# Performance work log

Hardware: AMD Instinct MI355X
Metric: run time of the kernel (lower is better)

The kernel has to match this reference:

```python
import jax, jax.numpy as jnp
import numpy as np

STRIDE = 1
PADDING = 1

def setup_inputs() -> dict:
    key = jax.random.key(0)
    k1, k2 = jax.random.split(key)
    x = jax.random.normal(k1, (32, 128, 56, 56), dtype=jnp.float32)
    # kaiming_uniform_(a=sqrt(5)) -> U(-bound, bound), bound = sqrt(6/((1+5)*fan_in)) = 1/sqrt(fan_in)
    fan_in = 128 * 3 * 3
    bound = 1.0 / np.sqrt(fan_in)
    weight = jax.random.uniform(k2, (256, 128, 3, 3), dtype=jnp.float32, minval=-bound, maxval=bound)
    bias = jnp.zeros((256,), dtype=jnp.float32)
    return {"x": x, "weight": weight, "bias": bias}

def reference(x, weight, bias):
    # Dense 2D convolution (cross-correlation, matching torch semantics), NCHW/OIHW.
    out = jax.lax.conv_general_dilated(
        x, weight,
        window_strides=(STRIDE, STRIDE),
        padding=[(PADDING, PADDING), (PADDING, PADDING)],
        dimension_numbers=("NCHW", "OIHW", "NCHW"),
    )
    return out + bias[None, :, None, None]
```

## Files before the change

### kernel.cpp

```cpp
#include <hip/hip_runtime.h>

typedef __bf16 bfvec8 __attribute__((ext_vector_type(8)));
typedef float f32x4 __attribute__((ext_vector_type(4)));
typedef unsigned short u16x8 __attribute__((ext_vector_type(8)));
typedef unsigned int u32;

constexpr int C_IN = 128, Wd = 56, Hd = 56, HW = 3136, K_OUT = 256, N_IMG = 32;
constexpr int KKTOT = 1152;
constexpr int WP = 58;
constexpr size_t XP_ELEMS = (size_t)N_IMG * WP * WP * C_IN;
constexpr size_t XP_BYTES = XP_ELEMS * 2;
constexpr size_t WT_ELEMS = (size_t)9 * 4 * 2 * 128 * 32;

constexpr int HALO_BLKS = 456;
constexpr int WT_BLKS   = 1152;
constexpr int XPOSE_BLKS = N_IMG * Hd;
constexpr int PREP_GRID = HALO_BLKS + WT_BLKS + XPOSE_BLKS;

__device__ inline unsigned short f2bf(float f) {
    union { float f; unsigned u; } v; v.f = f;
    unsigned u = v.u;
    u += 0x7fffu + ((u >> 16) & 1u);
    return (unsigned short)(u >> 16);
}

__device__ inline void gld16(const void* g, void* l) {
    __builtin_amdgcn_global_load_lds(
        (const __attribute__((address_space(1))) u32*)g,
        (__attribute__((address_space(3))) u32*)l, 16, 0, 0);
}

#define CFENCE() asm volatile("" ::: "memory")

__global__ __launch_bounds__(256) void prep(const float* __restrict__ x,
                                            const float* __restrict__ wgt,
                                            unsigned short* __restrict__ xp,
                                            unsigned short* __restrict__ wt) {
    __shared__ unsigned short T[Wd * C_IN];
    const int bx = blockIdx.x;

    if (bx < HALO_BLKS) {
        int v = bx * 256 + threadIdx.x;
        int n = v / 3648, rem = v - n * 3648;
        int p = rem >> 4, c8 = rem & 15;
        int hh, ww;
        if (p < 58)       { hh = 0;       ww = p;       }
        else if (p < 116) { hh = 57;      ww = p - 58;  }
        else if (p < 172) { hh = p - 115; ww = 0;       }
        else              { hh = p - 171; ww = 57;      }
        const u16x8 z = {0, 0, 0, 0, 0, 0, 0, 0};
        *(u16x8*)(xp + ((size_t)(n * WP + hh) * WP + ww) * C_IN + c8 * 8) = z;
        return;
    }
    if (bx < HALO_BLKS + WT_BLKS) {
        int o = (bx - HALO_BLKS) * 256 + threadIdx.x;
        int kk = o & 31, n = (o >> 5) & 127, nt = (o >> 12) & 1,
            ch = (o >> 13) & 3, rs = o >> 15;
        float v = wgt[(size_t)(nt * 128 + n) * KKTOT + (ch * 32 + kk) * 9 + rs];
        wt[o] = f2bf(v);
        return;
    }
    const int nb = bx - (HALO_BLKS + WT_BLKS);
    const int n = nb / Hd, h = nb - n * Hd;
    const float* src = x + (size_t)n * C_IN * HW + h * Wd;
    #pragma unroll
    for (int k = 0; k < 7; ++k) {
        int idx = threadIdx.x + k * 256;
        int c = idx / 14, w4 = idx - c * 14;
        const float4 v = *(const float4*)(src + (size_t)c * HW + w4 * 4);
        const int sw = (w4 & 15) * 8;
        T[(w4 * 4 + 0) * C_IN + (c ^ sw)] = f2bf(v.x);
        T[(w4 * 4 + 1) * C_IN + (c ^ sw)] = f2bf(v.y);
        T[(w4 * 4 + 2) * C_IN + (c ^ sw)] = f2bf(v.z);
        T[(w4 * 4 + 3) * C_IN + (c ^ sw)] = f2bf(v.w);
    }
    __syncthreads();
    unsigned short* dst = xp + ((size_t)(n * WP + h + 1) * WP + 1) * C_IN;
    const u16x8* s8 = (const u16x8*)T;
    u16x8* d8 = (u16x8*)dst;
    #pragma unroll
    for (int k = 0; k < 4; ++k) {
        int idx = threadIdx.x + k * 256;
        if (idx < 896) {
            int w = idx >> 4, j8 = idx & 15;
            d8[idx] = s8[w * 16 + (j8 ^ ((w >> 2) & 15))];
        }
    }
}

__global__ __launch_bounds__(256) void conv_gemm(
    const unsigned short* __restrict__ xp, const unsigned short* __restrict__ wt,
    const float* __restrict__ bias, float* __restrict__ out)
{
    __shared__ __align__(16) unsigned short As[3][128 * 32];

    const int tid = threadIdx.x;
    const int hbx = blockIdx.x;
    const int lbx = (hbx & 7) * 196 + (hbx >> 3);
    const int nt  = lbx & 1;
    const int mtile = (lbx >> 1) * 128;

    const int cg8 = ((tid & 3) ^ ((tid >> 3) & 3)) * 8;

    const unsigned short *gA0, *gA1;
    {
        int mrow = tid >> 2;
        int m = mtile + mrow;
        int ni = m / HW; int hw = m - ni * HW; int h = hw / Wd; int w = hw - h * Wd;
        gA0 = xp + ((size_t)(ni * WP + h + 1) * WP + (w + 1)) * C_IN + cg8;
        m += 64;
        ni = m / HW; hw = m - ni * HW; h = hw / Wd; w = hw - h * Wd;
        gA1 = xp + ((size_t)(ni * WP + h + 1) * WP + (w + 1)) * C_IN + cg8;
    }

    const int wave = tid >> 6, lane = tid & 63;
    const int wrow = (wave >> 1) * 64, wcol = (wave & 1) * 64;
    const int r16 = lane & 15, quad = lane >> 4;
    const int qsw = (quad ^ ((r16 >> 1) & 3)) * 8;

    const unsigned short* gBf = wt + (size_t)nt * 4096 + (wcol + r16) * 32 + quad * 8;

    const f32x4 zero4 = {0.f, 0.f, 0.f, 0.f};
    f32x4 acc[4][4];
    #pragma unroll
    for (int i = 0; i < 4; ++i)
        #pragma unroll
        for (int j = 0; j < 4; ++j)
            acc[i][j] = zero4;

    bfvec8 bf[2][4];

    auto issueA = [&](int step, int buf) {
        const int rs = step >> 2, ch = step & 3;
        const int dr = rs / 3 - 1, dc = rs % 3 - 1;
        const int aoff = (dr * WP + dc) * C_IN + ch * 32;
        gld16(gA0 + aoff, (void*)(As[buf] + tid * 8));
        gld16(gA1 + aoff, (void*)(As[buf] + 2048 + tid * 8));
    };
    auto loadB = [&](int step, int par) {
        #pragma unroll
        for (int ni = 0; ni < 4; ++ni)
            bf[par][ni] = *(const bfvec8*)(gBf + (size_t)step * 8192 + ni * 512);
    };

    issueA(0, 0);
    loadB(0, 0);
    issueA(1, 1);

    #pragma unroll
    for (int step = 0; step < 36; ++step) {
        const int cur = step % 3;
        const int par = step & 1;

        CFENCE(); __builtin_amdgcn_s_barrier(); CFENCE();
        if (step < 35) loadB(step + 1, par ^ 1);
        if (step < 34) issueA(step + 2, (step + 2) % 3);
        if (step < 34) {
            asm volatile("s_waitcnt vmcnt(8)" ::: "memory");
        } else if (step == 34) {
            asm volatile("s_waitcnt vmcnt(4)" ::: "memory");
        } else {
            asm volatile("s_waitcnt vmcnt(0)" ::: "memory");
        }
        CFENCE(); __builtin_amdgcn_s_barrier(); CFENCE();

        bfvec8 af[4];
        #pragma unroll
        for (int mi = 0; mi < 4; ++mi)
            af[mi] = *(const bfvec8*)&As[cur][(wrow + mi * 16 + r16) * 32 + qsw];

        #pragma unroll
        for (int mi = 0; mi < 4; ++mi)
            #pragma unroll
            for (int ni = 0; ni < 4; ++ni)
                acc[mi][ni] = __builtin_amdgcn_mfma_f32_16x16x32_bf16(
                    af[mi], bf[par][ni], acc[mi][ni], 0, 0, 0);
    }

    const int ntile = nt * 128;
    #pragma unroll
    for (int ni = 0; ni < 4; ++ni) {
        const int k = ntile + wcol + ni * 16 + r16;
        const float bb = bias[k];
        #pragma unroll
        for (int mi = 0; mi < 4; ++mi) {
            const int mb  = mtile + wrow + mi * 16 + quad * 4;
            const int ne  = mb / HW;
            const int hwe = mb - ne * HW;
            f32x4 v;
            #pragma unroll
            for (int i = 0; i < 4; ++i) v[i] = acc[mi][ni][i] + bb;
            *(f32x4*)(out + ((size_t)ne * K_OUT + k) * HW + hwe) = v;
        }
    }
}

extern "C" void kernel_launch(void* const* d_in, const int* in_sizes, int n_in,
                              void* d_out, int out_size, void* d_ws, size_t ws_size,
                              hipStream_t stream) {
    const float* x    = (const float*)d_in[0];
    const float* wgt  = (const float*)d_in[1];
    const float* bias = (const float*)d_in[2];
    float* out = (float*)d_out;

    unsigned short* xp = (unsigned short*)d_ws;
    unsigned short* wt = (unsigned short*)((char*)d_ws + XP_BYTES);

    prep<<<dim3(PREP_GRID), dim3(256), 0, stream>>>(x, wgt, xp, wt);
    conv_gemm<<<dim3(1568), dim3(256), 0, stream>>>(xp, wt, bias, out);
}
```

Baseline: 225.4 us.

## Enlarge GEMM tile to 256x128 and stage weights through LDS

Doubles the M tile per block from 128 to 256 rows, so each wave computes 128x64 with 8x4 MFMA accumulators, and halves the grid to 784 blocks. Weight tiles are now loaded into LDS with async global-to-LDS copies alongside the activations, instead of each wave loading them directly into registers. This is meant to increase arithmetic intensity and cut redundant weight fetches. In exchange it doubles accumulator registers and raises LDS use, with 784 blocks on 256 CUs risking uneven tail utilization.

After: 217.1 us. 1.04x faster.

```diff
diff --git a/kernel.cpp b/kernel.cpp
--- a/kernel.cpp
+++ b/kernel.cpp
@@ -88,93 +88,86 @@
     }
 }
 
-__global__ __launch_bounds__(256) void conv_gemm(
+__global__ __launch_bounds__(256, 2) void conv_gemm(
     const unsigned short* __restrict__ xp, const unsigned short* __restrict__ wt,
     const float* __restrict__ bias, float* __restrict__ out)
 {
-    __shared__ __align__(16) unsigned short As[3][128 * 32];
+    __shared__ __align__(16) unsigned short As[3][256 * 32];
+    __shared__ __align__(16) unsigned short Bs[3][128 * 32];
 
     const int tid = threadIdx.x;
     const int hbx = blockIdx.x;
-    const int lbx = (hbx & 7) * 196 + (hbx >> 3);
+    const int lbx = (hbx & 7) * 98 + (hbx >> 3);
     const int nt  = lbx & 1;
-    const int mtile = (lbx >> 1) * 128;
+    const int mtile = (lbx >> 1) * 256;
 
     const int cg8 = ((tid & 3) ^ ((tid >> 3) & 3)) * 8;
 
-    const unsigned short *gA0, *gA1;
-    {
-        int mrow = tid >> 2;
-        int m = mtile + mrow;
+    const unsigned short* gA[4];
+    #pragma unroll
+    for (int L = 0; L < 4; ++L) {
+        int m = mtile + L * 64 + (tid >> 2);
         int ni = m / HW; int hw = m - ni * HW; int h = hw / Wd; int w = hw - h * Wd;
-        gA0 = xp + ((size_t)(ni * WP + h + 1) * WP + (w + 1)) * C_IN + cg8;
-        m += 64;
-        ni = m / HW; hw = m - ni * HW; h = hw / Wd; w = hw - h * Wd;
-        gA1 = xp + ((size_t)(ni * WP + h + 1) * WP + (w + 1)) * C_IN + cg8;
-    }
+        gA[L] = xp + ((size_t)(ni * WP + h + 1) * WP + (w + 1)) * C_IN + cg8;
+    }
+    const unsigned short* gB = wt + (size_t)nt * 4096 + (size_t)(tid & 0xFC) * 8 + cg8;
 
     const int wave = tid >> 6, lane = tid & 63;
-    const int wrow = (wave >> 1) * 64, wcol = (wave & 1) * 64;
+    const int wrow = (wave >> 1) * 128, wcol = (wave & 1) * 64;
     const int r16 = lane & 15, quad = lane >> 4;
     const int qsw = (quad ^ ((r16 >> 1) & 3)) * 8;
 
-    const unsigned short* gBf = wt + (size_t)nt * 4096 + (wcol + r16) * 32 + quad * 8;
-
     const f32x4 zero4 = {0.f, 0.f, 0.f, 0.f};
-    f32x4 acc[4][4];
-    #pragma unroll
-    for (int i = 0; i < 4; ++i)
+    f32x4 acc[8][4];
+    #pragma unroll
+    for (int i = 0; i < 8; ++i)
         #pragma unroll
         for (int j = 0; j < 4; ++j)
             acc[i][j] = zero4;
 
-    bfvec8 bf[2][4];
-
-    auto issueA = [&](int step, int buf) {
+    auto issue = [&](int step, int buf) {
         const int rs = step >> 2, ch = step & 3;
         const int dr = rs / 3 - 1, dc = rs % 3 - 1;
         const int aoff = (dr * WP + dc) * C_IN + ch * 32;
-        gld16(gA0 + aoff, (void*)(As[buf] + tid * 8));
-        gld16(gA1 + aoff, (void*)(As[buf] + 2048 + tid * 8));
+        const size_t boff = (size_t)step * 8192;
+        #pragma unroll
+        for (int L = 0; L < 4; ++L)
+            gld16(gA[L] + aoff, (void*)(As[buf] + L * 2048 + tid * 8));
+        gld16(gB + boff,        (void*)(Bs[buf] + tid * 8));
+        gld16(gB + boff + 2048, (void*)(Bs[buf] + 2048 + tid * 8));
     };
-    auto loadB = [&](int step, int par) {
-        #pragma unroll
-        for (int ni = 0; ni < 4; ++ni)
-            bf[par][ni] = *(const bfvec8*)(gBf + (size_t)step * 8192 + ni * 512);
-    };
-
-    issueA(0, 0);
-    loadB(0, 0);
-    issueA(1, 1);
+
+    issue(0, 0);
+    issue(1, 1);
 
     #pragma unroll
     for (int step = 0; step < 36; ++step) {
         const int cur = step % 3;
-        const int par = step & 1;
 
         CFENCE(); __builtin_amdgcn_s_barrier(); CFENCE();
-        if (step < 35) loadB(step + 1, par ^ 1);
-        if (step < 34) issueA(step + 2, (step + 2) % 3);
         if (step < 34) {
-            asm volatile("s_waitcnt vmcnt(8)" ::: "memory");
+            issue(step + 2, (step + 2) % 3);
+            asm volatile("s_waitcnt vmcnt(12)" ::: "memory");
         } else if (step == 34) {
-            asm volatile("s_waitcnt vmcnt(4)" ::: "memory");
+            asm volatile("s_waitcnt vmcnt(6)" ::: "memory");
         } else {
             asm volatile("s_waitcnt vmcnt(0)" ::: "memory");
         }
         CFENCE(); __builtin_amdgcn_s_barrier(); CFENCE();
 
-        bfvec8 af[4];
-        #pragma unroll
-        for (int mi = 0; mi < 4; ++mi)
-            af[mi] = *(const bfvec8*)&As[cur][(wrow + mi * 16 + r16) * 32 + qsw];
-
-        #pragma unroll
-        for (int mi = 0; mi < 4; ++mi)
+        bfvec8 bf[4];
+        #pragma unroll
+        for (int ni = 0; ni < 4; ++ni)
+            bf[ni] = *(const bfvec8*)&Bs[cur][(wcol + ni * 16 + r16) * 32 + qsw];
+
+        #pragma unroll
+        for (int mi = 0; mi < 8; ++mi) {
+            const bfvec8 af = *(const bfvec8*)&As[cur][(wrow + mi * 16 + r16) * 32 + qsw];
             #pragma unroll
             for (int ni = 0; ni < 4; ++ni)
                 acc[mi][ni] = __builtin_amdgcn_mfma_f32_16x16x32_bf16(
-                    af[mi], bf[par][ni], acc[mi][ni], 0, 0, 0);
+                    af, bf[ni], acc[mi][ni], 0, 0, 0);
+        }
     }
 
     const int ntile = nt * 128;
@@ -183,7 +176,7 @@
         const int k = ntile + wcol + ni * 16 + r16;
         const float bb = bias[k];
         #pragma unroll
-        for (int mi = 0; mi < 4; ++mi) {
+        for (int mi = 0; mi < 8; ++mi) {
             const int mb  = mtile + wrow + mi * 16 + quad * 4;
             const int ne  = mb / HW;
             const int hwe = mb - ne * HW;
@@ -207,5 +200,5 @@
     unsigned short* wt = (unsigned short*)((char*)d_ws + XP_BYTES);
 
     prep<<<dim3(PREP_GRID), dim3(256), 0, stream>>>(x, wgt, xp, wt);
-    conv_gemm<<<dim3(1568), dim3(256), 0, stream>>>(xp, wt, bias, out);
-}
+    conv_gemm<<<dim3(784), dim3(256), 0, stream>>>(xp, wt, bias, out);
+}
```

## Stage weight tiles through LDS and double-buffer fragment reads ahead of MFMA

Applied to the files above, without the earlier changes.

The weight (B) operand was loaded per lane directly from global memory. It now goes through a triple-buffered LDS tile using async global_load_lds, matching how A is loaded. Fragments for the next step are read from LDS before the current step's MFMAs, and the MFMA block runs at raised wave priority via s_setprio. Launch bounds now request 3 blocks per SM. The goal is fewer redundant global B loads and better overlap of LDS reads with matrix math, at the cost of double the LDS footprint and more registers for the doubled A fragments.

Result: faster. 214.8 us (-4.7%).

```diff
diff --git a/kernel.cpp b/kernel.cpp
--- a/kernel.cpp
+++ b/kernel.cpp
@@ -88,11 +88,12 @@
     }
 }
 
-__global__ __launch_bounds__(256) void conv_gemm(
+__global__ __launch_bounds__(256, 3) void conv_gemm(
     const unsigned short* __restrict__ xp, const unsigned short* __restrict__ wt,
     const float* __restrict__ bias, float* __restrict__ out)
 {
     __shared__ __align__(16) unsigned short As[3][128 * 32];
+    __shared__ __align__(16) unsigned short Bs[3][128 * 32];
 
     const int tid = threadIdx.x;
     const int hbx = blockIdx.x;
@@ -112,14 +113,13 @@
         ni = m / HW; hw = m - ni * HW; h = hw / Wd; w = hw - h * Wd;
         gA1 = xp + ((size_t)(ni * WP + h + 1) * WP + (w + 1)) * C_IN + cg8;
     }
+    const unsigned short* gB = wt + (size_t)nt * 4096 + (size_t)(tid & 0xFC) * 8 + cg8;
 
     const int wave = tid >> 6, lane = tid & 63;
     const int wrow = (wave >> 1) * 64, wcol = (wave & 1) * 64;
     const int r16 = lane & 15, quad = lane >> 4;
     const int qsw = (quad ^ ((r16 >> 1) & 3)) * 8;
 
-    const unsigned short* gBf = wt + (size_t)nt * 4096 + (wcol + r16) * 32 + quad * 8;
-
     const f32x4 zero4 = {0.f, 0.f, 0.f, 0.f};
     f32x4 acc[4][4];
     #pragma unroll
@@ -128,53 +128,57 @@
         for (int j = 0; j < 4; ++j)
             acc[i][j] = zero4;
 
-    bfvec8 bf[2][4];
-
-    auto issueA = [&](int step, int buf) {
+    bfvec8 af[2][4], bf[2][4];
+
+    auto issue = [&](int step, int buf) {
         const int rs = step >> 2, ch = step & 3;
         const int dr = rs / 3 - 1, dc = rs % 3 - 1;
         const int aoff = (dr * WP + dc) * C_IN + ch * 32;
+        const size_t boff = (size_t)step * 8192;
         gld16(gA0 + aoff, (void*)(As[buf] + tid * 8));
         gld16(gA1 + aoff, (void*)(As[buf] + 2048 + tid * 8));
+        gld16(gB + boff,        (void*)(Bs[buf] + tid * 8));
+        gld16(gB + boff + 2048, (void*)(Bs[buf] + 2048 + tid * 8));
     };
-    auto loadB = [&](int step, int par) {
+    auto readFrags = [&](int step, int set) {
+        const int cur = step % 3;
+        #pragma unroll
+        for (int mi = 0; mi < 4; ++mi)
+            af[set][mi] = *(const bfvec8*)&As[cur][(wrow + mi * 16 + r16) * 32 + qsw];
         #pragma unroll
         for (int ni = 0; ni < 4; ++ni)
-            bf[par][ni] = *(const bfvec8*)(gBf + (size_t)step * 8192 + ni * 512);
+            bf[set][ni] = *(const bfvec8*)&Bs[cur][(wcol + ni * 16 + r16) * 32 + qsw];
     };
 
-    issueA(0, 0);
-    loadB(0, 0);
-    issueA(1, 1);
+    issue(0, 0);
+    issue(1, 1);
+    asm volatile("s_waitcnt vmcnt(4)" ::: "memory");
+    CFENCE(); __builtin_amdgcn_s_barrier(); CFENCE();
+    readFrags(0, 0);
 
     #pragma unroll
     for (int step = 0; step < 36; ++step) {
-        const int cur = step % 3;
         const int par = step & 1;
 
         CFENCE(); __builtin_amdgcn_s_barrier(); CFENCE();
-        if (step < 35) loadB(step + 1, par ^ 1);
-        if (step < 34) issueA(step + 2, (step + 2) % 3);
         if (step < 34) {
-            asm volatile("s_waitcnt vmcnt(8)" ::: "memory");
+            issue(step + 2, (step + 2) % 3);
+            asm volatile("s_waitcnt vmcnt(4)" ::: "memory");
         } else if (step == 34) {
-            asm volatile("s_waitcnt vmcnt(4)" ::: "memory");
-        } else {
             asm volatile("s_waitcnt vmcnt(0)" ::: "memory");
         }
         CFENCE(); __builtin_amdgcn_s_barrier(); CFENCE();
 
-        bfvec8 af[4];
-        #pragma unroll
-        for (int mi = 0; mi < 4; ++mi)
-            af[mi] = *(const bfvec8*)&As[cur][(wrow + mi * 16 + r16) * 32 + qsw];
-
+        if (step < 35) readFrags(step + 1, par ^ 1);
+
+        __builtin_amdgcn_s_setprio(1);
         #pragma unroll
         for (int mi = 0; mi < 4; ++mi)
             #pragma unroll
             for (int ni = 0; ni < 4; ++ni)
                 acc[mi][ni] = __builtin_amdgcn_mfma_f32_16x16x32_bf16(
-                    af[mi], bf[par][ni], acc[mi][ni], 0, 0, 0);
+                    af[par][mi], bf[par][ni], acc[mi][ni], 0, 0, 0);
+        __builtin_amdgcn_s_setprio(0);
     }
 
     const int ntile = nt * 128;
```
